# Kernel tuning notes

Hardware: AMD Instinct MI355X
Metric: run time of the kernel (lower is better)

The kernel has to match this reference:

```python
import jax, jax.numpy as jnp
import numpy as np
from functools import partial

B, A = 256, 32          # batch_size, num_atoms
N = B * A               # total nodes = 8192
E = 262144              # edges
H = 128                 # hidden_dim
LD, AF = 64, 16         # latent_dim, atom_feature_dim
L = 6                   # num_layers
LN_EPS = 1e-5

silu = jax.nn.silu


def setup_inputs() -> dict:
    key = jax.random.key(0)
    ks = jax.random.split(key, 32)
    s = 0.02
    inp = {
        "z": jax.random.normal(ks[0], (B, LD), jnp.float32),
        "atom_types": jax.random.uniform(ks[1], (N, AF), jnp.float32),
        "pos_init": jax.random.normal(ks[2], (N, 3), jnp.float32) * 0.1,
        "edge_index": jax.random.randint(ks[3], (2, E), 0, N, jnp.int64) if jax.config.jax_enable_x64 else jax.random.randint(ks[3], (2, E), 0, N, jnp.int32),
        "batch": jax.random.randint(ks[4], (N,), 0, B, jnp.int32),
        # latent injector: (LD+AF)->2H -> 2H->H -> H->H
        "inj_W1": jax.random.normal(ks[5], (LD + AF, 2 * H), jnp.float32) * s,
        "inj_b1": jnp.zeros((2 * H,), jnp.float32),
        "inj_W2": jax.random.normal(ks[6], (2 * H, H), jnp.float32) * s,
        "inj_b2": jnp.zeros((H,), jnp.float32),
        "inj_W3": jax.random.normal(ks[7], (H, H), jnp.float32) * s,
        "inj_b3": jnp.zeros((H,), jnp.float32),
        # stacked per-layer params [L, ...]
        "edge_W1": jax.random.normal(ks[8], (L, 2 * H + 1, H), jnp.float32) * s,
        "edge_b1": jnp.zeros((L, H), jnp.float32),
        "edge_W2": jax.random.normal(ks[9], (L, H, H), jnp.float32) * s,
        "edge_b2": jnp.zeros((L, H), jnp.float32),
        "node_W1": jax.random.normal(ks[10], (L, 2 * H, H), jnp.float32) * s,
        "node_b1": jnp.zeros((L, H), jnp.float32),
        "node_W2": jax.random.normal(ks[11], (L, H, H), jnp.float32) * s,
        "node_b2": jnp.zeros((L, H), jnp.float32),
        "coord_W1": jax.random.normal(ks[12], (L, H, H), jnp.float32) * s,
        "coord_b1": jnp.zeros((L, H), jnp.float32),
        "coord_W2": jax.random.normal(ks[13], (L, H, 1), jnp.float32) * s,  # no bias
        "ln_g": jnp.ones((L, H), jnp.float32),
        "ln_b": jnp.zeros((L, H), jnp.float32),
    }
    return inp


def _layer_norm(x, g, b):
    mu = jnp.mean(x, axis=-1, keepdims=True)
    var = jnp.mean(jnp.square(x - mu), axis=-1, keepdims=True)
    return (x - mu) * jax.lax.rsqrt(var + LN_EPS) * g + b


def _egnn_forward(z, atom_types, pos_init, row, col,
                  inj_W1, inj_b1, inj_W2, inj_b2, inj_W3, inj_b3,
                  edge_W1, edge_b1, edge_W2, edge_b2,
                  node_W1, node_b1, node_W2, node_b2,
                  coord_W1, coord_b1, coord_W2, ln_g, ln_b):
    # latent injection
    z_exp = jnp.repeat(z, A, axis=0)                      # [N, LD]
    h0 = jnp.concatenate([atom_types, z_exp], axis=1)     # [N, AF+LD]
    h = silu(h0 @ inj_W1 + inj_b1)
    h = silu(h @ inj_W2 + inj_b2)
    h = h @ inj_W3 + inj_b3                               # [N, H]

    deg = jax.ops.segment_sum(jnp.ones((E,), h.dtype), row, num_segments=N)[:, None]  # [N,1]

    def step(carry, p):
        h, pos = carry
        (eW1, eb1, eW2, eb2, nW1, nb1, nW2, nb2, cW1, cb1, cW2, g, b) = p
        dpos = pos[row] - pos[col]                                   # [E,3]
        dist_sq = jnp.sum(jnp.square(dpos), axis=1, keepdims=True)   # [E,1]
        ef = jnp.concatenate([h[row], h[col], dist_sq], axis=1)      # [E,2H+1]
        m = silu(silu(ef @ eW1 + eb1) @ eW2 + eb2)                   # [E,H]
        cw = silu(m @ cW1 + cb1) @ cW2                               # [E,1]
        coord_update = jax.ops.segment_sum(cw * dpos, row, num_segments=N)  # [N,3]
        pos_new = pos + coord_update / (deg + 1e-6)
        agg = jax.ops.segment_sum(m, row, num_segments=N)            # [N,H]
        nu = silu(jnp.concatenate([h, agg], axis=1) @ nW1 + nb1) @ nW2 + nb2
        h_new = _layer_norm(h + nu, g, b)
        return (h_new, pos_new), None

    params = (edge_W1, edge_b1, edge_W2, edge_b2, node_W1, node_b1,
              node_W2, node_b2, coord_W1, coord_b1, coord_W2, ln_g, ln_b)
    (h, pos), _ = jax.lax.scan(step, (h, pos_init), params)
    return pos


def reference(z, atom_types, pos_init, edge_index, batch,
              inj_W1, inj_b1, inj_W2, inj_b2, inj_W3, inj_b3,
              edge_W1, edge_b1, edge_W2, edge_b2,
              node_W1, node_b1, node_W2, node_b2,
              coord_W1, coord_b1, coord_W2, ln_g, ln_b):
    row, col = edge_index[0], edge_index[1]
    return _egnn_forward(z, atom_types, pos_init, row, col,
                         inj_W1, inj_b1, inj_W2, inj_b2, inj_W3, inj_b3,
                         edge_W1, edge_b1, edge_W2, edge_b2,
                         node_W1, node_b1, node_W2, node_b2,
                         coord_W1, coord_b1, coord_W2, ln_g, ln_b)
```

## Files before the change

kernel.cpp:

```cpp
#include <hip/hip_runtime.h>
#include <hip/hip_bf16.h>

#define NNODES 8192
#define NEDGES 262144
#define HDIM 128
#define NLAYERS 6
#define NMASK (NNODES - 1)

typedef __attribute__((ext_vector_type(8))) short bf16x8;
typedef __attribute__((ext_vector_type(4))) float f32x4;
typedef const __attribute__((address_space(1))) void gvoid;
typedef __attribute__((address_space(3))) void svoid;

__device__ __forceinline__ float silu_f(float x) {
    return x * __builtin_amdgcn_rcpf(1.0f + __expf(-x));
}
__device__ __forceinline__ unsigned short f2bu(float x) {
    unsigned int u; __builtin_memcpy(&u, &x, 4);
    return (unsigned short)((u + 0x8000u) >> 16);
}
__device__ __forceinline__ float bu2f(unsigned short u) {
    unsigned int v = ((unsigned int)u) << 16;
    float f; __builtin_memcpy(&f, &v, 4);
    return f;
}

__device__ __forceinline__ void stage_slice(const unsigned short* src,
                                            unsigned short* dst, int w) {
    const unsigned short* s = src + w * 1024;
    unsigned short* d = dst + w * 1024;
    __builtin_amdgcn_global_load_lds((gvoid*)s, (svoid*)d, 16, 0, 0);
    __builtin_amdgcn_global_load_lds((gvoid*)(s + 512), (svoid*)(d + 512), 16, 0, 0);
}

__global__ void detect_kernel(const int* __restrict__ ei32, int* __restrict__ flags) {
    if (blockIdx.x == 0 && threadIdx.x == 0) {
        flags[1] = (ei32[1] == 0 && ei32[3] == 0 && ei32[5] == 0 && ei32[7] == 0) ? 1 : 0;
    }
}
__device__ __forceinline__ int load_idx(const void* ei, int is64, int i) {
    int v = is64 ? (int)(((const long long*)ei)[i]) : ((const int*)ei)[i];
    return v & NMASK;
}

__global__ void pos_init_kernel(const float* __restrict__ pin, float* __restrict__ pos) {
    int i = blockIdx.x * blockDim.x + threadIdx.x;
    if (i < NNODES * 3) pos[i] = pin[i];
}

__global__ void cnt_kernel(const void* __restrict__ ei, const int* __restrict__ flags,
                           int* __restrict__ cnt) {
    int i = blockIdx.x * blockDim.x + threadIdx.x;
    if (i < NEDGES) atomicAdd(&cnt[load_idx(ei, flags[1], i)], 1);
}
__global__ void scan_kernel(const int* __restrict__ cnt, int* __restrict__ woff,
                            float* __restrict__ deg) {
    __shared__ int sums[256];
    const int t = threadIdx.x;
    const int base = t * 32;
    int s = 0;
#pragma unroll
    for (int i = 0; i < 32; ++i) s += cnt[base + i];
    sums[t] = s;
    __syncthreads();
    if (t == 0) {
        int run = 0;
        for (int k = 0; k < 256; ++k) { int v = sums[k]; sums[k] = run; run += v; }
    }
    __syncthreads();
    int run = sums[t];
#pragma unroll
    for (int i = 0; i < 32; ++i) {
        int c = cnt[base + i];
        woff[base + i] = run;
        deg[base + i] = (float)c;
        run += c;
    }
}
__global__ void scatter_kernel(const void* __restrict__ ei, const int* __restrict__ flags,
                               int* __restrict__ woff,
                               int* __restrict__ rowS, int* __restrict__ colS) {
    int i = blockIdx.x * blockDim.x + threadIdx.x;
    if (i < NEDGES) {
        const int is64 = flags[1];
        int r = load_idx(ei, is64, i);
        int c = load_idx(ei, is64, NEDGES + i);
        int p = atomicAdd(&woff[r], 1);
        rowS[p] = r;
        colS[p] = c;
    }
}

__global__ void prep_weights_kernel(const float* __restrict__ eW1,
                                    const float* __restrict__ eW2,
                                    const float* __restrict__ cW1,
                                    const float* __restrict__ nW1,
                                    const float* __restrict__ nW2,
                                    unsigned short* __restrict__ w1tb,
                                    unsigned short* __restrict__ w2tb,
                                    unsigned short* __restrict__ c1tb,
                                    unsigned short* __restrict__ n1tb,
                                    unsigned short* __restrict__ n2tb,
                                    float* __restrict__ w1d) {
    const int TB = NLAYERS * 8 * 4 * 128 * 8;
    const int TS = NLAYERS * 4 * 4 * 128 * 8;
    const int TD = NLAYERS * 128;
    const int TOT = 2 * TB + 3 * TS + TD;
    for (int i = blockIdx.x * blockDim.x + threadIdx.x; i < TOT;
         i += gridDim.x * blockDim.x) {
        if (i < TB) {
            int j = i & 7, r = i >> 3;
            int n = r & 127; r >>= 7;
            int ch = r & 3; r >>= 2;
            int sl = r & 7; int l = r >> 3;
            int k = sl * 32 + ch * 8 + j;
            w1tb[i] = f2bu(eW1[((size_t)l * 257 + k) * 128 + n]);
        } else if (i < TB + TS) {
            int q = i - TB;
            int j = q & 7, r = q >> 3;
            int n = r & 127; r >>= 7;
            int ch = r & 3; r >>= 2;
            int sl = r & 3; int l = r >> 2;
            int k = sl * 32 + ch * 8 + j;
            w2tb[q] = f2bu(eW2[((size_t)l * 128 + k) * 128 + n]);
        } else if (i < TB + 2 * TS) {
            int q = i - TB - TS;
            int j = q & 7, r = q >> 3;
            int n = r & 127; r >>= 7;
            int ch = r & 3; r >>= 2;
            int sl = r & 3; int l = r >> 2;
            int k = sl * 32 + ch * 8 + j;
            c1tb[q] = f2bu(cW1[((size_t)l * 128 + k) * 128 + n]);
        } else if (i < 2 * TB + 2 * TS) {
            int q = i - TB - 2 * TS;
            int j = q & 7, r = q >> 3;
            int n = r & 127; r >>= 7;
            int ch = r & 3; r >>= 2;
            int sl = r & 7; int l = r >> 3;
            int k = sl * 32 + ch * 8 + j;
            n1tb[q] = f2bu(nW1[((size_t)l * 256 + k) * 128 + n]);
        } else if (i < 2 * TB + 3 * TS) {
            int q = i - 2 * TB - 2 * TS;
            int j = q & 7, r = q >> 3;
            int n = r & 127; r >>= 7;
            int ch = r & 3; r >>= 2;
            int sl = r & 3; int l = r >> 2;
            int k = sl * 32 + ch * 8 + j;
            n2tb[q] = f2bu(nW2[((size_t)l * 128 + k) * 128 + n]);
        } else {
            int r = i - 2 * TB - 3 * TS, l = r / 128, n = r % 128;
            w1d[r] = eW1[((size_t)l * 257 + 256) * 128 + n];
        }
    }
}

__global__ __launch_bounds__(256) void inj_kernel(
    const float* __restrict__ atom, const float* __restrict__ z,
    const float* __restrict__ W1, const float* __restrict__ b1,
    const float* __restrict__ W2, const float* __restrict__ b2,
    const float* __restrict__ W3, const float* __restrict__ b3,
    unsigned short* __restrict__ hb)
{
    __shared__ __align__(16) float in_s[16][84];
    __shared__ __align__(16) float s1[16][260];
    __shared__ __align__(16) float s2[16][132];
    const int tid = threadIdx.x;
    const int n0 = blockIdx.x * 16;

    if (tid < 80) {
        for (int e = 0; e < 16; ++e) {
            int n = n0 + e;
            in_s[e][tid] = (tid < 16) ? atom[n * 16 + tid] : z[(n >> 5) * 64 + (tid - 16)];
        }
    }
    __syncthreads();
    {
        float acc[16];
        float bias = b1[tid];
#pragma unroll
        for (int e = 0; e < 16; ++e) acc[e] = bias;
        for (int k4 = 0; k4 < 20; ++k4) {
            float w0 = W1[(k4 * 4 + 0) * 256 + tid];
            float w1 = W1[(k4 * 4 + 1) * 256 + tid];
            float w2 = W1[(k4 * 4 + 2) * 256 + tid];
            float w3 = W1[(k4 * 4 + 3) * 256 + tid];
#pragma unroll
            for (int e = 0; e < 16; ++e) {
                const float4 v = *(const float4*)&in_s[e][k4 * 4];
                acc[e] += v.x * w0 + v.y * w1 + v.z * w2 + v.w * w3;
            }
        }
#pragma unroll
        for (int e = 0; e < 16; ++e) s1[e][tid] = silu_f(acc[e]);
    }
    __syncthreads();
    const int j = tid & 127, hv = tid >> 7;
    {
        float acc[8];
        float bias = b2[j];
#pragma unroll
        for (int e = 0; e < 8; ++e) acc[e] = bias;
        for (int k4 = 0; k4 < 64; ++k4) {
            float w0 = W2[(k4 * 4 + 0) * 128 + j];
            float w1 = W2[(k4 * 4 + 1) * 128 + j];
            float w2 = W2[(k4 * 4 + 2) * 128 + j];
            float w3 = W2[(k4 * 4 + 3) * 128 + j];
#pragma unroll
            for (int e = 0; e < 8; ++e) {
                const float4 v = *(const float4*)&s1[hv * 8 + e][k4 * 4];
                acc[e] += v.x * w0 + v.y * w1 + v.z * w2 + v.w * w3;
            }
        }
#pragma unroll
        for (int e = 0; e < 8; ++e) s2[hv * 8 + e][j] = silu_f(acc[e]);
    }
    __syncthreads();
    {
        float acc[8];
        float bias = b3[j];
#pragma unroll
        for (int e = 0; e < 8; ++e) acc[e] = bias;
        for (int k4 = 0; k4 < 32; ++k4) {
            float w0 = W3[(k4 * 4 + 0) * 128 + j];
            float w1 = W3[(k4 * 4 + 1) * 128 + j];
            float w2 = W3[(k4 * 4 + 2) * 128 + j];
            float w3 = W3[(k4 * 4 + 3) * 128 + j];
#pragma unroll
            for (int e = 0; e < 8; ++e) {
                const float4 v = *(const float4*)&s2[hv * 8 + e][k4 * 4];
                acc[e] += v.x * w0 + v.y * w1 + v.z * w2 + v.w * w3;
            }
        }
#pragma unroll
        for (int e = 0; e < 8; ++e)
            hb[(size_t)(n0 + hv * 8 + e) * HDIM + j] = f2bu(acc[e]);
    }
}

__global__ __launch_bounds__(256, 3) void edge_mfma_kernel(
    const unsigned short* __restrict__ hb, const float* __restrict__ pos,
    const int* __restrict__ rowS, const int* __restrict__ colS,
    const unsigned short* __restrict__ w1tb,
    const unsigned short* __restrict__ w2tb,
    const unsigned short* __restrict__ c1tb,
    const float* __restrict__ w1d,
    const float* __restrict__ eb1, const float* __restrict__ eb2,
    const float* __restrict__ cb1, const float* __restrict__ cw2,
    float* __restrict__ agg, float* __restrict__ cu)
{
    __shared__ __align__(16) unsigned short Cbuf[128][136];
    __shared__ __align__(16) unsigned short Bbuf[4096];

    const int tid = threadIdx.x;
    const int e0 = blockIdx.x * 128;
    const int L = tid & 63, w = tid >> 6;
    const int quad = L >> 4, l16 = L & 15;
    const int m0 = w * 32;

    stage_slice(w1tb, Bbuf, w);

    if (tid < 128) {
        int r = rowS[e0 + tid], c = colS[e0 + tid];
        float dx = pos[r * 3 + 0] - pos[c * 3 + 0];
        float dy = pos[r * 3 + 1] - pos[c * 3 + 1];
        float dz = pos[r * 3 + 2] - pos[c * 3 + 2];
        *(float*)&Cbuf[tid][128] = dx * dx + dy * dy + dz * dz;
        Cbuf[tid][130] = (unsigned short)r;
        Cbuf[tid][131] = (unsigned short)c;
        Cbuf[tid][132] = f2bu(dx); Cbuf[tid][133] = f2bu(dy); Cbuf[tid][134] = f2bu(dz);
    }
    __syncthreads();

    const int r0 = Cbuf[m0 + l16][130];
    const int r1 = Cbuf[m0 + 16 + l16][130];
    const int c0 = Cbuf[m0 + l16][131];
    const int c1 = Cbuf[m0 + 16 + l16][131];

    f32x4 acc[2][8];
    const f32x4 zero = {0.f, 0.f, 0.f, 0.f};

#pragma unroll
    for (int mt = 0; mt < 2; ++mt)
#pragma unroll
        for (int nt = 0; nt < 8; ++nt) acc[mt][nt] = zero;

#pragma unroll
    for (int kc = 0; kc < 8; ++kc) {
        const int kk = (kc & 3) * 32 + quad * 8;
        const int n0i = (kc < 4) ? r0 : c0;
        const int n1i = (kc < 4) ? r1 : c1;
        bf16x8 a0 = *(const bf16x8*)(hb + (size_t)n0i * HDIM + kk);
        bf16x8 a1 = *(const bf16x8*)(hb + (size_t)n1i * HDIM + kk);
        const unsigned short* bp = Bbuf + quad * 1024;
#pragma unroll
        for (int nt = 0; nt < 8; ++nt) {
            bf16x8 b = *(const bf16x8*)&bp[(nt * 16 + l16) * 8];
            acc[0][nt] = __builtin_amdgcn_mfma_f32_16x16x32_bf16(a0, b, acc[0][nt], 0, 0, 0);
            acc[1][nt] = __builtin_amdgcn_mfma_f32_16x16x32_bf16(a1, b, acc[1][nt], 0, 0, 0);
        }
        __syncthreads();
        stage_slice((kc < 7) ? w1tb + (kc + 1) * 4096 : w2tb, Bbuf, w);
        if (kc == 7) {
#pragma unroll
            for (int nt = 0; nt < 8; ++nt) {
                const int n = nt * 16 + l16;
                const float wd = w1d[n];
                const float bias = eb1[n];
#pragma unroll
                for (int mt = 0; mt < 2; ++mt)
#pragma unroll
                    for (int r = 0; r < 4; ++r) {
                        const int m = m0 + mt * 16 + quad * 4 + r;
                        float dsq = *(const float*)&Cbuf[m][128];
                        Cbuf[m][n] = f2bu(silu_f(acc[mt][nt][r] + bias + dsq * wd));
                    }
            }
        }
        __syncthreads();
    }

#pragma unroll
    for (int mt = 0; mt < 2; ++mt)
#pragma unroll
        for (int nt = 0; nt < 8; ++nt) acc[mt][nt] = zero;
#pragma unroll
    for (int kc = 0; kc < 4; ++kc) {
        const int kk = kc * 32 + quad * 8;
        bf16x8 a0 = *(const bf16x8*)&Cbuf[m0 + l16][kk];
        bf16x8 a1 = *(const bf16x8*)&Cbuf[m0 + 16 + l16][kk];
        const unsigned short* bp = Bbuf + quad * 1024;
#pragma unroll
        for (int nt = 0; nt < 8; ++nt) {
            bf16x8 b = *(const bf16x8*)&bp[(nt * 16 + l16) * 8];
            acc[0][nt] = __builtin_amdgcn_mfma_f32_16x16x32_bf16(a0, b, acc[0][nt], 0, 0, 0);
            acc[1][nt] = __builtin_amdgcn_mfma_f32_16x16x32_bf16(a1, b, acc[1][nt], 0, 0, 0);
        }
        __syncthreads();
        stage_slice((kc < 3) ? w2tb + (kc + 1) * 4096 : c1tb, Bbuf, w);
        if (kc == 3) {
#pragma unroll
            for (int nt = 0; nt < 8; ++nt) {
                const int n = nt * 16 + l16;
                const float bias = eb2[n];
#pragma unroll
                for (int mt = 0; mt < 2; ++mt)
#pragma unroll
                    for (int r = 0; r < 4; ++r) {
                        const int m = m0 + mt * 16 + quad * 4 + r;
                        Cbuf[m][n] = f2bu(silu_f(acc[mt][nt][r] + bias));
                    }
            }
        }
        __syncthreads();
    }

#pragma unroll
    for (int mt = 0; mt < 2; ++mt)
#pragma unroll
        for (int nt = 0; nt < 8; ++nt) acc[mt][nt] = zero;
#pragma unroll
    for (int kc = 0; kc < 4; ++kc) {
        const int kk = kc * 32 + quad * 8;
        bf16x8 a0 = *(const bf16x8*)&Cbuf[m0 + l16][kk];
        bf16x8 a1 = *(const bf16x8*)&Cbuf[m0 + 16 + l16][kk];
        const unsigned short* bp = Bbuf + quad * 1024;
#pragma unroll
        for (int nt = 0; nt < 8; ++nt) {
            bf16x8 b = *(const bf16x8*)&bp[(nt * 16 + l16) * 8];
            acc[0][nt] = __builtin_amdgcn_mfma_f32_16x16x32_bf16(a0, b, acc[0][nt], 0, 0, 0);
            acc[1][nt] = __builtin_amdgcn_mfma_f32_16x16x32_bf16(a1, b, acc[1][nt], 0, 0, 0);
        }
        if (kc < 3) {
            __syncthreads();
            stage_slice(c1tb + (kc + 1) * 4096, Bbuf, w);
            __syncthreads();
        }
    }
    {
        float s[2][4] = {{0.f, 0.f, 0.f, 0.f}, {0.f, 0.f, 0.f, 0.f}};
#pragma unroll
        for (int nt = 0; nt < 8; ++nt) {
            const int n = nt * 16 + l16;
            const float bias = cb1[n];
            const float wv = cw2[n];
#pragma unroll
            for (int mt = 0; mt < 2; ++mt)
#pragma unroll
                for (int r = 0; r < 4; ++r)
                    s[mt][r] += silu_f(acc[mt][nt][r] + bias) * wv;
        }
#pragma unroll
        for (int mt = 0; mt < 2; ++mt)
#pragma unroll
            for (int r = 0; r < 4; ++r) {
                float v = s[mt][r];
                v += __shfl_xor(v, 1);
                v += __shfl_xor(v, 2);
                v += __shfl_xor(v, 4);
                v += __shfl_xor(v, 8);
                if (l16 == 0)
                    *(float*)&Cbuf[m0 + mt * 16 + quad * 4 + r][128] = v;
            }
    }
    __syncthreads();

    if (tid < 3) {
        int curr = Cbuf[0][130];
        float s = 0.0f;
        for (int e = 0; e < 128; ++e) {
            int r = Cbuf[e][130];
            if (r != curr) { atomicAdd(&cu[curr * 3 + tid], s); s = 0.0f; curr = r; }
            s += *(const float*)&Cbuf[e][128] * bu2f(Cbuf[e][132 + tid]);
        }
        atomicAdd(&cu[curr * 3 + tid], s);
    }
    {
        const int q = tid >> 6;
        const int p = tid & 63;
        const int eb = q * 32;
        int curr = Cbuf[eb][130];
        float s0 = 0.0f, s1 = 0.0f;
#pragma unroll 4
        for (int i = 0; i < 32; ++i) {
            const int e = eb + i;
            int r = Cbuf[e][130];
            if (r != curr) {
                atomicAdd(&agg[(size_t)curr * HDIM + 2 * p], s0);
                atomicAdd(&agg[(size_t)curr * HDIM + 2 * p + 1], s1);
                s0 = 0.0f; s1 = 0.0f; curr = r;
            }
            unsigned int v = *(const unsigned int*)&Cbuf[e][2 * p];
            s0 += bu2f((unsigned short)(v & 0xffffu));
            s1 += bu2f((unsigned short)(v >> 16));
        }
        atomicAdd(&agg[(size_t)curr * HDIM + 2 * p], s0);
        atomicAdd(&agg[(size_t)curr * HDIM + 2 * p + 1], s1);
    }
}

__global__ __launch_bounds__(128) void node_mfma_kernel(
    const unsigned short* __restrict__ hb,
    float* __restrict__ agg,
    float* __restrict__ cu, const float* __restrict__ deg,
    const unsigned short* __restrict__ n1tb,
    const unsigned short* __restrict__ n2tb,
    const float* __restrict__ b1, const float* __restrict__ b2,
    const float* __restrict__ lg, const float* __restrict__ lb,
    unsigned short* __restrict__ h2b,
    float* __restrict__ pos)
{
    __shared__ __align__(16) unsigned short Cbuf[32][136];
    const int tid = threadIdx.x;
    const int n0 = blockIdx.x * 32;

    if (tid < 32) {
        int n = n0 + tid;
        float inv = __builtin_amdgcn_rcpf(deg[n] + 1e-6f);
        pos[n * 3 + 0] += cu[n * 3 + 0] * inv;
        pos[n * 3 + 1] += cu[n * 3 + 1] * inv;
        pos[n * 3 + 2] += cu[n * 3 + 2] * inv;
        cu[n * 3 + 0] = 0.0f;
        cu[n * 3 + 1] = 0.0f;
        cu[n * 3 + 2] = 0.0f;
    }

    const int L = tid & 63, w = tid >> 6;
    const int quad = L >> 4, l16 = L & 15;
    const int m0 = w * 16;
    const int row = n0 + m0 + l16;

    f32x4 acc[8];
    const f32x4 zero = {0.f, 0.f, 0.f, 0.f};

#pragma unroll
    for (int nt = 0; nt < 8; ++nt) acc[nt] = zero;
#pragma unroll
    for (int kc = 0; kc < 8; ++kc) {
        bf16x8 a;
        if (kc < 4) {
            const int kk = kc * 32 + quad * 8;
            a = *(const bf16x8*)(hb + (size_t)row * HDIM + kk);
        } else {
            const int kk = (kc - 4) * 32 + quad * 8;
            const float4* p = (const float4*)(agg + (size_t)row * HDIM + kk);
            float4 u0 = p[0], u1 = p[1];
            a[0] = (short)f2bu(u0.x); a[1] = (short)f2bu(u0.y);
            a[2] = (short)f2bu(u0.z); a[3] = (short)f2bu(u0.w);
            a[4] = (short)f2bu(u1.x); a[5] = (short)f2bu(u1.y);
            a[6] = (short)f2bu(u1.z); a[7] = (short)f2bu(u1.w);
        }
        const unsigned short* bp = n1tb + ((kc * 4 + quad) * 128) * 8;
#pragma unroll
        for (int nt = 0; nt < 8; ++nt) {
            bf16x8 b = *(const bf16x8*)(bp + (nt * 16 + l16) * 8);
            acc[nt] = __builtin_amdgcn_mfma_f32_16x16x32_bf16(a, b, acc[nt], 0, 0, 0);
        }
    }
    {
        const float4 z4 = {0.f, 0.f, 0.f, 0.f};
        float4* ap = (float4*)(agg + (size_t)row * HDIM + quad * 32);
#pragma unroll
        for (int i = 0; i < 8; ++i) ap[i] = z4;
    }
#pragma unroll
    for (int nt = 0; nt < 8; ++nt) {
        const int n = nt * 16 + l16;
        const float bias = b1[n];
#pragma unroll
        for (int r = 0; r < 4; ++r) {
            const int m = m0 + quad * 4 + r;
            Cbuf[m][n] = f2bu(silu_f(acc[nt][r] + bias));
        }
    }

#pragma unroll
    for (int nt = 0; nt < 8; ++nt) acc[nt] = zero;
#pragma unroll
    for (int kc = 0; kc < 4; ++kc) {
        const int kk = kc * 32 + quad * 8;
        bf16x8 a = *(const bf16x8*)&Cbuf[m0 + l16][kk];
        const unsigned short* bp = n2tb + ((kc * 4 + quad) * 128) * 8;
#pragma unroll
        for (int nt = 0; nt < 8; ++nt) {
            bf16x8 b = *(const bf16x8*)(bp + (nt * 16 + l16) * 8);
            acc[nt] = __builtin_amdgcn_mfma_f32_16x16x32_bf16(a, b, acc[nt], 0, 0, 0);
        }
    }

#pragma unroll
    for (int nt = 0; nt < 8; ++nt) {
        const int n = nt * 16 + l16;
        const float bias = b2[n];
#pragma unroll
        for (int r = 0; r < 4; ++r) {
            const int m = m0 + quad * 4 + r;
            acc[nt][r] += bias + bu2f(hb[(size_t)(n0 + m) * HDIM + n]);
        }
    }
    float mu[4], rs[4];
#pragma unroll
    for (int r = 0; r < 4; ++r) {
        float s = 0.0f, ss = 0.0f;
#pragma unroll
        for (int nt = 0; nt < 8; ++nt) {
            float x = acc[nt][r];
            s += x; ss += x * x;
        }
#pragma unroll
        for (int d = 1; d < 16; d <<= 1) {
            s += __shfl_xor(s, d);
            ss += __shfl_xor(ss, d);
        }
        float m_ = s * (1.0f / 128.0f);
        float var = ss * (1.0f / 128.0f) - m_ * m_;
        mu[r] = m_;
        rs[r] = rsqrtf(fmaxf(var, 0.0f) + 1e-5f);
    }
#pragma unroll
    for (int nt = 0; nt < 8; ++nt) {
        const int n = nt * 16 + l16;
        const float gg = lg[n], bb = lb[n];
#pragma unroll
        for (int r = 0; r < 4; ++r) {
            const int m = m0 + quad * 4 + r;
            float val = (acc[nt][r] - mu[r]) * rs[r] * gg + bb;
            h2b[(size_t)(n0 + m) * HDIM + n] = f2bu(val);
        }
    }
}

extern "C" void kernel_launch(void* const* d_in, const int* in_sizes, int n_in,
                              void* d_out, int out_size, void* d_ws, size_t ws_size,
                              hipStream_t stream) {
    const float* zF    = (const float*)d_in[0];
    const float* atomF = (const float*)d_in[1];
    const float* posI  = (const float*)d_in[2];
    const void*  ei    = d_in[3];
    const float* iW1 = (const float*)d_in[5];  const float* ib1 = (const float*)d_in[6];
    const float* iW2 = (const float*)d_in[7];  const float* ib2 = (const float*)d_in[8];
    const float* iW3 = (const float*)d_in[9];  const float* ib3 = (const float*)d_in[10];
    const float* eW1 = (const float*)d_in[11]; const float* eb1 = (const float*)d_in[12];
    const float* eW2 = (const float*)d_in[13]; const float* eb2 = (const float*)d_in[14];
    const float* nW1 = (const float*)d_in[15]; const float* nb1 = (const float*)d_in[16];
    const float* nW2 = (const float*)d_in[17]; const float* nb2 = (const float*)d_in[18];
    const float* cW1 = (const float*)d_in[19]; const float* cb1 = (const float*)d_in[20];
    const float* cW2 = (const float*)d_in[21];
    const float* lng = (const float*)d_in[22]; const float* lnb = (const float*)d_in[23];

    float* pos = (float*)d_out;

    float* ws = (float*)d_ws;
    int* flags = (int*)d_ws;
    size_t cur = 16;
    auto carve = [&](size_t n) { float* p = ws + cur; cur += n; return p; };
    float* deg  = carve(NNODES);
    float* cu   = carve((size_t)NNODES * 3);
    float* agg  = carve((size_t)NNODES * HDIM);
    unsigned short* hbA = (unsigned short*)carve((size_t)NNODES * HDIM / 2);
    unsigned short* hbB = (unsigned short*)carve((size_t)NNODES * HDIM / 2);
    unsigned short* w1tb = (unsigned short*)carve((size_t)NLAYERS * 8 * 4096 / 2);
    unsigned short* w2tb = (unsigned short*)carve((size_t)NLAYERS * 4 * 4096 / 2);
    unsigned short* c1tb = (unsigned short*)carve((size_t)NLAYERS * 4 * 4096 / 2);
    unsigned short* n1tb = (unsigned short*)carve((size_t)NLAYERS * 8 * 4096 / 2);
    unsigned short* n2tb = (unsigned short*)carve((size_t)NLAYERS * 4 * 4096 / 2);
    float* w1d  = carve(NLAYERS * 128);
    int* cnt    = (int*)carve(NNODES);
    int* woff   = (int*)carve(NNODES);
    int* rowS   = (int*)carve(NEDGES);
    int* colS   = (int*)carve(NEDGES);

    detect_kernel<<<1, 64, 0, stream>>>((const int*)ei, flags);
    pos_init_kernel<<<(NNODES * 3 + 255) / 256, 256, 0, stream>>>(posI, pos);

    hipMemsetAsync(cnt, 0, NNODES * sizeof(int), stream);
    cnt_kernel<<<NEDGES / 256, 256, 0, stream>>>(ei, flags, cnt);
    scan_kernel<<<1, 256, 0, stream>>>(cnt, woff, deg);
    scatter_kernel<<<NEDGES / 256, 256, 0, stream>>>(ei, flags, woff, rowS, colS);

    prep_weights_kernel<<<2691, 256, 0, stream>>>(eW1, eW2, cW1, nW1, nW2,
                                                  w1tb, w2tb, c1tb, n1tb, n2tb, w1d);
    inj_kernel<<<NNODES / 16, 256, 0, stream>>>(atomF, zF, iW1, ib1, iW2, ib2, iW3, ib3,
                                                hbA);

    hipMemsetAsync(agg, 0, (size_t)NNODES * HDIM * sizeof(float), stream);
    hipMemsetAsync(cu, 0, (size_t)NNODES * 3 * sizeof(float), stream);

    unsigned short* hb = hbA;
    unsigned short* ob = hbB;
    for (int l = 0; l < NLAYERS; ++l) {
        edge_mfma_kernel<<<NEDGES / 128, 256, 0, stream>>>(
            hb, pos, rowS, colS,
            w1tb + (size_t)l * 8 * 4096,
            w2tb + (size_t)l * 4 * 4096,
            c1tb + (size_t)l * 4 * 4096,
            w1d + (size_t)l * 128,
            eb1 + l * 128, eb2 + l * 128, cb1 + l * 128, cW2 + l * 128,
            agg, cu);
        node_mfma_kernel<<<NNODES / 32, 128, 0, stream>>>(
            hb, agg, cu, deg,
            n1tb + (size_t)l * 8 * 4096,
            n2tb + (size_t)l * 4 * 4096,
            nb1 + l * 128, nb2 + l * 128,
            lng + l * 128, lnb + l * 128,
            ob, pos);
        unsigned short* tb = hb; hb = ob; ob = tb;
    }
}
```

Measured before the change: 778.5 us.

## Double-buffer edge weight slices and prefetch gathered node features into registers

Packs the three per-layer edge weight matrices into one contiguous slice array and runs all 16 MFMA k-slices in a single loop. Weight slices are staged into a double-buffered LDS area, so the next slice loads while the current one is consumed, using one barrier per slice instead of two. All row and column node-feature gathers are issued up front into registers rather than once per k-chunk. This raises LDS use by 8 KB per block and register pressure from 16 held bf16x8 vectors, which could reduce occupancy under launch_bounds(256,3).

New measurement: 794.1 us. Within noise of the previous version (+2.0%).

```diff
diff --git a/kernel.cpp b/kernel.cpp
--- a/kernel.cpp
+++ b/kernel.cpp
@@ -96,9 +96,7 @@
                                     const float* __restrict__ cW1,
                                     const float* __restrict__ nW1,
                                     const float* __restrict__ nW2,
-                                    unsigned short* __restrict__ w1tb,
-                                    unsigned short* __restrict__ w2tb,
-                                    unsigned short* __restrict__ c1tb,
+                                    unsigned short* __restrict__ ewt,
                                     unsigned short* __restrict__ n1tb,
                                     unsigned short* __restrict__ n2tb,
                                     float* __restrict__ w1d) {
@@ -114,7 +112,8 @@
             int ch = r & 3; r >>= 2;
             int sl = r & 7; int l = r >> 3;
             int k = sl * 32 + ch * 8 + j;
-            w1tb[i] = f2bu(eW1[((size_t)l * 257 + k) * 128 + n]);
+            ewt[(size_t)(l * 16 + sl) * 4096 + ch * 1024 + n * 8 + j] =
+                f2bu(eW1[((size_t)l * 257 + k) * 128 + n]);
         } else if (i < TB + TS) {
             int q = i - TB;
             int j = q & 7, r = q >> 3;
@@ -122,7 +121,8 @@
             int ch = r & 3; r >>= 2;
             int sl = r & 3; int l = r >> 2;
             int k = sl * 32 + ch * 8 + j;
-            w2tb[q] = f2bu(eW2[((size_t)l * 128 + k) * 128 + n]);
+            ewt[(size_t)(l * 16 + 8 + sl) * 4096 + ch * 1024 + n * 8 + j] =
+                f2bu(eW2[((size_t)l * 128 + k) * 128 + n]);
         } else if (i < TB + 2 * TS) {
             int q = i - TB - TS;
             int j = q & 7, r = q >> 3;
@@ -130,7 +130,8 @@
             int ch = r & 3; r >>= 2;
             int sl = r & 3; int l = r >> 2;
             int k = sl * 32 + ch * 8 + j;
-            c1tb[q] = f2bu(cW1[((size_t)l * 128 + k) * 128 + n]);
+            ewt[(size_t)(l * 16 + 12 + sl) * 4096 + ch * 1024 + n * 8 + j] =
+                f2bu(cW1[((size_t)l * 128 + k) * 128 + n]);
         } else if (i < 2 * TB + 2 * TS) {
             int q = i - TB - 2 * TS;
             int j = q & 7, r = q >> 3;
@@ -240,16 +241,14 @@
 __global__ __launch_bounds__(256, 3) void edge_mfma_kernel(
     const unsigned short* __restrict__ hb, const float* __restrict__ pos,
     const int* __restrict__ rowS, const int* __restrict__ colS,
-    const unsigned short* __restrict__ w1tb,
-    const unsigned short* __restrict__ w2tb,
-    const unsigned short* __restrict__ c1tb,
+    const unsigned short* __restrict__ wt,
     const float* __restrict__ w1d,
     const float* __restrict__ eb1, const float* __restrict__ eb2,
     const float* __restrict__ cb1, const float* __restrict__ cw2,
     float* __restrict__ agg, float* __restrict__ cu)
 {
     __shared__ __align__(16) unsigned short Cbuf[128][136];
-    __shared__ __align__(16) unsigned short Bbuf[4096];
+    __shared__ __align__(16) unsigned short Bbuf[2][4096];
 
     const int tid = threadIdx.x;
     const int e0 = blockIdx.x * 128;
@@ -257,7 +256,7 @@
     const int quad = L >> 4, l16 = L & 15;
     const int m0 = w * 32;
 
-    stage_slice(w1tb, Bbuf, w);
+    stage_slice(wt, Bbuf[0], w);
 
     if (tid < 128) {
         int r = rowS[e0 + tid], c = colS[e0 + tid];
@@ -276,31 +275,47 @@
     const int c0 = Cbuf[m0 + l16][131];
     const int c1 = Cbuf[m0 + 16 + l16][131];
 
+    bf16x8 aR0[4], aR1[4], aC0[4], aC1[4];
+#pragma unroll
+    for (int kc = 0; kc < 4; ++kc) {
+        const int kk = kc * 32 + quad * 8;
+        aR0[kc] = *(const bf16x8*)(hb + (size_t)r0 * HDIM + kk);
+        aR1[kc] = *(const bf16x8*)(hb + (size_t)r1 * HDIM + kk);
+        aC0[kc] = *(const bf16x8*)(hb + (size_t)c0 * HDIM + kk);
+        aC1[kc] = *(const bf16x8*)(hb + (size_t)c1 * HDIM + kk);
+    }
+
     f32x4 acc[2][8];
     const f32x4 zero = {0.f, 0.f, 0.f, 0.f};
-
 #pragma unroll
     for (int mt = 0; mt < 2; ++mt)
 #pragma unroll
         for (int nt = 0; nt < 8; ++nt) acc[mt][nt] = zero;
 
 #pragma unroll
-    for (int kc = 0; kc < 8; ++kc) {
-        const int kk = (kc & 3) * 32 + quad * 8;
-        const int n0i = (kc < 4) ? r0 : c0;
-        const int n1i = (kc < 4) ? r1 : c1;
-        bf16x8 a0 = *(const bf16x8*)(hb + (size_t)n0i * HDIM + kk);
-        bf16x8 a1 = *(const bf16x8*)(hb + (size_t)n1i * HDIM + kk);
-        const unsigned short* bp = Bbuf + quad * 1024;
+    for (int s = 0; s < 16; ++s) {
+        if (s) __syncthreads();
+        if (s < 15) stage_slice(wt + (s + 1) * 4096, Bbuf[(s + 1) & 1], w);
+
+        const unsigned short* bp = Bbuf[s & 1] + quad * 1024;
+        bf16x8 a0, a1;
+        if (s < 4) {
+            a0 = aR0[s]; a1 = aR1[s];
+        } else if (s < 8) {
+            a0 = aC0[s - 4]; a1 = aC1[s - 4];
+        } else {
+            const int kk = ((s - 8) & 3) * 32 + quad * 8;
+            a0 = *(const bf16x8*)&Cbuf[m0 + l16][kk];
+            a1 = *(const bf16x8*)&Cbuf[m0 + 16 + l16][kk];
+        }
 #pragma unroll
         for (int nt = 0; nt < 8; ++nt) {
             bf16x8 b = *(const bf16x8*)&bp[(nt * 16 + l16) * 8];
             acc[0][nt] = __builtin_amdgcn_mfma_f32_16x16x32_bf16(a0, b, acc[0][nt], 0, 0, 0);
             acc[1][nt] = __builtin_amdgcn_mfma_f32_16x16x32_bf16(a1, b, acc[1][nt], 0, 0, 0);
         }
-        __syncthreads();
-        stage_slice((kc < 7) ? w1tb + (kc + 1) * 4096 : w2tb, Bbuf, w);
-        if (kc == 7) {
+
+        if (s == 7) {
 #pragma unroll
             for (int nt = 0; nt < 8; ++nt) {
                 const int n = nt * 16 + l16;
@@ -315,29 +330,11 @@
                         Cbuf[m][n] = f2bu(silu_f(acc[mt][nt][r] + bias + dsq * wd));
                     }
             }
-        }
-        __syncthreads();
-    }
-
-#pragma unroll
-    for (int mt = 0; mt < 2; ++mt)
-#pragma unroll
-        for (int nt = 0; nt < 8; ++nt) acc[mt][nt] = zero;
-#pragma unroll
-    for (int kc = 0; kc < 4; ++kc) {
-        const int kk = kc * 32 + quad * 8;
-        bf16x8 a0 = *(const bf16x8*)&Cbuf[m0 + l16][kk];
-        bf16x8 a1 = *(const bf16x8*)&Cbuf[m0 + 16 + l16][kk];
-        const unsigned short* bp = Bbuf + quad * 1024;
-#pragma unroll
-        for (int nt = 0; nt < 8; ++nt) {
-            bf16x8 b = *(const bf16x8*)&bp[(nt * 16 + l16) * 8];
-            acc[0][nt] = __builtin_amdgcn_mfma_f32_16x16x32_bf16(a0, b, acc[0][nt], 0, 0, 0);
-            acc[1][nt] = __builtin_amdgcn_mfma_f32_16x16x32_bf16(a1, b, acc[1][nt], 0, 0, 0);
-        }
-        __syncthreads();
-        stage_slice((kc < 3) ? w2tb + (kc + 1) * 4096 : c1tb, Bbuf, w);
-        if (kc == 3) {
+#pragma unroll
+            for (int mt = 0; mt < 2; ++mt)
+#pragma unroll
+                for (int nt = 0; nt < 8; ++nt) acc[mt][nt] = zero;
+        } else if (s == 11) {
 #pragma unroll
             for (int nt = 0; nt < 8; ++nt) {
                 const int n = nt * 16 + l16;
@@ -350,32 +347,13 @@
                         Cbuf[m][n] = f2bu(silu_f(acc[mt][nt][r] + bias));
                     }
             }
-        }
-        __syncthreads();
-    }
-
-#pragma unroll
-    for (int mt = 0; mt < 2; ++mt)
-#pragma unroll
-        for (int nt = 0; nt < 8; ++nt) acc[mt][nt] = zero;
-#pragma unroll
-    for (int kc = 0; kc < 4; ++kc) {
-        const int kk = kc * 32 + quad * 8;
-        bf16x8 a0 = *(const bf16x8*)&Cbuf[m0 + l16][kk];
-        bf16x8 a1 = *(const bf16x8*)&Cbuf[m0 + 16 + l16][kk];
-        const unsigned short* bp = Bbuf + quad * 1024;
-#pragma unroll
-        for (int nt = 0; nt < 8; ++nt) {
-            bf16x8 b = *(const bf16x8*)&bp[(nt * 16 + l16) * 8];
-            acc[0][nt] = __builtin_amdgcn_mfma_f32_16x16x32_bf16(a0, b, acc[0][nt], 0, 0, 0);
-            acc[1][nt] = __builtin_amdgcn_mfma_f32_16x16x32_bf16(a1, b, acc[1][nt], 0, 0, 0);
-        }
-        if (kc < 3) {
-            __syncthreads();
-            stage_slice(c1tb + (kc + 1) * 4096, Bbuf, w);
-            __syncthreads();
-        }
-    }
+#pragma unroll
+            for (int mt = 0; mt < 2; ++mt)
+#pragma unroll
+                for (int nt = 0; nt < 8; ++nt) acc[mt][nt] = zero;
+        }
+    }
+
     {
         float s[2][4] = {{0.f, 0.f, 0.f, 0.f}, {0.f, 0.f, 0.f, 0.f}};
 #pragma unroll
@@ -598,9 +576,7 @@
     float* agg  = carve((size_t)NNODES * HDIM);
     unsigned short* hbA = (unsigned short*)carve((size_t)NNODES * HDIM / 2);
     unsigned short* hbB = (unsigned short*)carve((size_t)NNODES * HDIM / 2);
-    unsigned short* w1tb = (unsigned short*)carve((size_t)NLAYERS * 8 * 4096 / 2);
-    unsigned short* w2tb = (unsigned short*)carve((size_t)NLAYERS * 4 * 4096 / 2);
-    unsigned short* c1tb = (unsigned short*)carve((size_t)NLAYERS * 4 * 4096 / 2);
+    unsigned short* ewt  = (unsigned short*)carve((size_t)NLAYERS * 16 * 4096 / 2);
     unsigned short* n1tb = (unsigned short*)carve((size_t)NLAYERS * 8 * 4096 / 2);
     unsigned short* n2tb = (unsigned short*)carve((size_t)NLAYERS * 4 * 4096 / 2);
     float* w1d  = carve(NLAYERS * 128);
@@ -618,7 +594,7 @@
     scatter_kernel<<<NEDGES / 256, 256, 0, stream>>>(ei, flags, woff, rowS, colS);
 
     prep_weights_kernel<<<2691, 256, 0, stream>>>(eW1, eW2, cW1, nW1, nW2,
-                                                  w1tb, w2tb, c1tb, n1tb, n2tb, w1d);
+                                                  ewt, n1tb, n2tb, w1d);
     inj_kernel<<<NNODES / 16, 256, 0, stream>>>(atomF, zF, iW1, ib1, iW2, ib2, iW3, ib3,
                                                 hbA);
 
@@ -630,9 +606,7 @@
     for (int l = 0; l < NLAYERS; ++l) {
         edge_mfma_kernel<<<NEDGES / 128, 256, 0, stream>>>(
             hb, pos, rowS, colS,
-            w1tb + (size_t)l * 8 * 4096,
-            w2tb + (size_t)l * 4 * 4096,
-            c1tb + (size_t)l * 4 * 4096,
+            ewt + (size_t)l * 16 * 4096,
             w1d + (size_t)l * 128,
             eb1 + l * 128, eb2 + l * 128, cb1 + l * 128, cW2 + l * 128,
             agg, cu);
```
